# Kernel optimization log

Measured on AMD Instinct MI355X. Metric: run time of the kernel, lower is better.

Reference implementation:

```python
import jax, jax.numpy as jnp
import numpy as np

N_WAY = 5
K_SHOT = 5
SEQ = 196          # patch tokens per image (ViT-S/16 @ 224)
TEMP = 0.0510310363  # similarity temperature ~ 1/sqrt(384)
LR = 0.1
OPT_STEPS = 15


def _normalize(emb):
    # [B, S, D] -> [B*S, D], rows L2-normalized with 1e-8 floor (matches torch.max(norm, 1e-8))
    v = emb.reshape(-1, emb.shape[-1])
    n = jnp.linalg.norm(v, axis=1, keepdims=True)
    return v / jnp.maximum(n, 1e-8)


def _block_mask():
    # block_diag of (SEQ x SEQ) blocks of -100 for each of the n_way*k_shot support images
    return jnp.kron(jnp.eye(N_WAY * K_SHOT, dtype=jnp.float32),
                    jnp.ones((SEQ, SEQ), jnp.float32)) * (-100.0)


def _predict(sup, qry, v, mask):
    # sup: [n_way*k_shot, S, D], qry: [Qb, Qs, D], v: [n_way*k_shot*S]
    S = sup.shape[1]
    Qb, Qs = qry.shape[0], qry.shape[1]
    C = _normalize(sup) @ _normalize(qry).T           # [Ls, Qb*Qs] cosine sims
    if mask is not None:
        C = C + mask
    pred = C + v[:, None]
    pred = pred.reshape(N_WAY, K_SHOT * S, Qb, Qs)
    pred = pred.transpose(0, 1, 3, 2).reshape(N_WAY, K_SHOT * S * Qs, Qb)
    pred = pred / TEMP
    pred = jax.scipy.special.logsumexp(pred, axis=1)  # [n_way, Qb]
    return pred.T                                     # [Qb, n_way]


def _optimize_v(sup_key, sup_query, labels, mask):
    # online SGD on the patch-embedding importance vector v (starts at zero)
    Ls = N_WAY * K_SHOT * sup_key.shape[1]
    B = sup_query.shape[0]

    def loss(v):
        p = _predict(sup_key, sup_query, v, mask)  # [B, n_way]
        logp = jax.nn.log_softmax(p, axis=1)
        return -jnp.mean(logp[jnp.arange(B), labels])

    def step(v, _):
        return v - LR * jax.grad(loss)(v), None

    v, _ = jax.lax.scan(step, jnp.zeros((Ls,), jnp.float32), None, length=OPT_STEPS)
    return v


def setup_inputs() -> dict:
    key = jax.random.key(0)
    k1, k2, k3, k4 = jax.random.split(key, 4)
    return {
        "support_emb_key": jax.random.normal(k1, (N_WAY * K_SHOT, SEQ, 384), jnp.float32),
        "support_emb_query": jax.random.normal(k2, (N_WAY * K_SHOT, SEQ, 384), jnp.float32),
        "query_emb": jax.random.normal(k3, (75, SEQ, 384), jnp.float32),
        "support_labels": jax.random.randint(k4, (N_WAY * K_SHOT,), 0, N_WAY, dtype=jnp.int32),
    }


def reference(support_emb_key, support_emb_query, query_emb, support_labels):
    mask = _block_mask()
    v = _optimize_v(support_emb_key, support_emb_query, support_labels, mask)
    return _predict(support_emb_key, query_emb, v, None)  # [75, n_way]
```

## Files before the change

kernel.cpp:

```cpp
#include <hip/hip_runtime.h>
#include <hip/hip_bf16.h>

#define NW 5
#define KS 5
#define SEQ 196
#define DIM 384
#define NSUP 25
#define NQRY 75
#define NIMG 100
#define LSUP 4900
#define LSUP_PAD 4992
#define QROWS 208
#define BLOCK_W 980
#define OPT_STEPS 15
#define MTILES 39
#define NSUPWG (NSUP * MTILES)
#define NQWG   (NQRY * MTILES)
#define SPIN_LIMIT (1u << 22)

static constexpr float TEMP_F = 0.0510310363f;
static constexpr float INV_T  = 1.0f / TEMP_F;
static constexpr float LR_F   = 0.1f;

typedef short v8s __attribute__((ext_vector_type(8)));
typedef float v4f __attribute__((ext_vector_type(4)));

__device__ inline unsigned short f2bf(float x) {
    unsigned int u = __float_as_uint(x);
    u += 0x7fffu + ((u >> 16) & 1u);
    return (unsigned short)(u >> 16);
}

__device__ __forceinline__ float fresh_f32(float* p) {
    return __hip_atomic_fetch_add(p, 0.0f, __ATOMIC_RELAXED, __HIP_MEMORY_SCOPE_AGENT);
}
__device__ __forceinline__ int fresh_i32(int* p) {
    return __hip_atomic_fetch_add(p, 0, __ATOMIC_RELAXED, __HIP_MEMORY_SCOPE_AGENT);
}
__device__ __forceinline__ unsigned fresh_u32(unsigned* p) {
    return __hip_atomic_fetch_add(p, 0u, __ATOMIC_RELAXED, __HIP_MEMORY_SCOPE_AGENT);
}
__device__ __forceinline__ void agent_store_f32(float* p, float v) {
    __hip_atomic_store(p, v, __ATOMIC_RELAXED, __HIP_MEMORY_SCOPE_AGENT);
}
__device__ __forceinline__ void agent_store_i32(int* p, int v) {
    __hip_atomic_store(p, v, __ATOMIC_RELAXED, __HIP_MEMORY_SCOPE_AGENT);
}

__global__ __launch_bounds__(256) void norm_all(const float* __restrict__ supk,
                                                const float* __restrict__ supq,
                                                const float* __restrict__ qry,
                                                unsigned short* __restrict__ Kb,
                                                unsigned short* __restrict__ Qall) {
    int R = blockIdx.x * 4 + (threadIdx.x >> 6);
    int l = threadIdx.x & 63;
    unsigned short* out;
    const float* in;
    float scale;
    if (R < LSUP_PAD) {
        out = Kb + (size_t)R * DIM;
        if (R >= LSUP) {
            #pragma unroll
            for (int k = 0; k < 6; ++k) out[l + 64 * k] = 0;
            return;
        }
        in = supk + (size_t)R * DIM;
        scale = INV_T;
    } else {
        int i = R - LSUP_PAD;
        int img = i / QROWS;
        int r = i - img * QROWS;
        out = Qall + (size_t)i * DIM;
        if (r >= SEQ) {
            #pragma unroll
            for (int k = 0; k < 6; ++k) out[l + 64 * k] = 0;
            return;
        }
        in = (img < NSUP)
            ? supq + ((size_t)img * SEQ + r) * DIM
            : qry  + ((size_t)(img - NSUP) * SEQ + r) * DIM;
        scale = 1.0f;
    }
    float x[6];
    #pragma unroll
    for (int k = 0; k < 6; ++k) x[k] = in[l + 64 * k];
    float s = 0.f;
    #pragma unroll
    for (int k = 0; k < 6; ++k) s += x[k] * x[k];
    #pragma unroll
    for (int m = 1; m < 64; m <<= 1) s += __shfl_xor(s, m);
    float sc = scale / fmaxf(sqrtf(s), 1e-8f);
    #pragma unroll
    for (int k = 0; k < 6; ++k) out[l + 64 * k] = f2bf(x[k] * sc);
}

#define MT  128
#define NTP 208
#define KCC 64

__device__ __forceinline__ void gload16(const void* g, void* l) {
    __builtin_amdgcn_global_load_lds(
        (__attribute__((address_space(1))) void*)g,
        (__attribute__((address_space(3))) void*)l, 16, 0, 0);
}

template<int IMG_BASE, int NWG, bool SUPPORT>
__device__ __forceinline__ void gemm_body(
    int gid,
    const unsigned short* __restrict__ Kb,
    const unsigned short* __restrict__ Qall,
    float* __restrict__ Rall,
    unsigned* counter,
    unsigned short* Asm, unsigned short* Bsm)
{
    int t = threadIdx.x;

    constexpr int qq = NWG >> 3;
    constexpr int rr = NWG & 7;
    int xcd = gid & 7;
    int sub = gid >> 3;
    int L = (xcd < rr ? xcd * (qq + 1) : rr * (qq + 1) + (xcd - rr) * qq) + sub;
    int img = IMG_BASE + L / MTILES;
    int m_base = (L % MTILES) * MT;

    const unsigned short* Qimg = Qall + (size_t)img * (QROWS * DIM);

    int wv = t >> 6;
    int l  = t & 63;
    int lo = l & 15;
    int hi = l >> 4;
    int mh = (wv >> 1) * 64;
    int nh = wv & 1;

    int srow = l >> 3;
    int skp  = (l & 7) ^ srow;
    const unsigned short* aSrc = Kb   + (size_t)(m_base + wv * 32 + srow) * DIM + skp * 8;
    const unsigned short* bSrc = Qimg + (size_t)srow * DIM + skp * 8;

    v4f acc[4][7];
    #pragma unroll
    for (int m = 0; m < 4; ++m)
        #pragma unroll
        for (int n = 0; n < 7; ++n)
            acc[m][n] = (v4f){0.f, 0.f, 0.f, 0.f};

    for (int kb = 0; kb < DIM; kb += KCC) {
        #pragma unroll
        for (int j = 0; j < 4; ++j)
            gload16(aSrc + (size_t)j * 8 * DIM + kb,
                    Asm + (wv * 32 + j * 8) * KCC);
        #pragma unroll
        for (int jj = 0; jj < 7; ++jj) {
            int j = wv + jj * 4;
            if (j < 26)
                gload16(bSrc + (size_t)j * 8 * DIM + kb,
                        Bsm + j * 8 * KCC);
        }
        __syncthreads();

        const unsigned short* Ar = Asm + (mh + lo) * KCC;
        const unsigned short* Br = Bsm + (nh * 112 + lo) * KCC;
        #pragma unroll
        for (int kk = 0; kk < 2; ++kk) {
            int koff = ((hi + 4 * kk) ^ (lo & 7)) * 8;
            v8s a0 = *(const v8s*)(Ar + koff);
            v8s a1 = *(const v8s*)(Ar + 16 * KCC + koff);
            v8s a2 = *(const v8s*)(Ar + 32 * KCC + koff);
            v8s a3 = *(const v8s*)(Ar + 48 * KCC + koff);
            #pragma unroll
            for (int n = 0; n < 7; ++n) {
                if (nh == 0 || n < 6) {
                    v8s bb = *(const v8s*)(Br + n * 16 * KCC + koff);
                    acc[0][n] = __builtin_amdgcn_mfma_f32_16x16x32_bf16(a0, bb, acc[0][n], 0, 0, 0);
                    acc[1][n] = __builtin_amdgcn_mfma_f32_16x16x32_bf16(a1, bb, acc[1][n], 0, 0, 0);
                    acc[2][n] = __builtin_amdgcn_mfma_f32_16x16x32_bf16(a2, bb, acc[2][n], 0, 0, 0);
                    acc[3][n] = __builtin_amdgcn_mfma_f32_16x16x32_bf16(a3, bb, acc[3][n], 0, 0, 0);
                }
            }
        }
        __syncthreads();
    }

    float s[4][4];
    #pragma unroll
    for (int m = 0; m < 4; ++m)
        #pragma unroll
        for (int j = 0; j < 4; ++j) s[m][j] = 0.f;
    #pragma unroll
    for (int n = 0; n < 7; ++n) {
        if (nh == 0 || n < 6) {
            bool ok = ((nh * 7 + n) * 16 + lo) < SEQ;
            #pragma unroll
            for (int m = 0; m < 4; ++m)
                #pragma unroll
                for (int j = 0; j < 4; ++j)
                    s[m][j] += ok ? __expf(acc[m][n][j]) : 0.f;
        }
    }
    #pragma unroll
    for (int mm = 1; mm < 16; mm <<= 1) {
        #pragma unroll
        for (int m = 0; m < 4; ++m)
            #pragma unroll
            for (int j = 0; j < 4; ++j)
                s[m][j] += __shfl_xor(s[m][j], mm);
    }
    float* rp = (float*)Asm;
    if (lo == 0) {
        #pragma unroll
        for (int m = 0; m < 4; ++m)
            #pragma unroll
            for (int j = 0; j < 4; ++j)
                rp[nh * 128 + mh + m * 16 + hi * 4 + j] = s[m][j];
    }
    __syncthreads();
    if (t < MT) {
        int gr = m_base + t;
        if (gr < LSUP) {
            float o = rp[t] + rp[128 + t];
            if (img < NSUP && (gr / SEQ) == img) o = 0.f;
            if (SUPPORT)
                agent_store_f32(&Rall[(size_t)img * LSUP + gr], o);
            else
                Rall[(size_t)img * LSUP + gr] = o;
        }
    }
    if (SUPPORT) {
        __syncthreads();
        if (t == 0)
            __hip_atomic_fetch_add(counter, 1u, __ATOMIC_RELAXED, __HIP_MEMORY_SCOPE_AGENT);
    }
}

__global__ __launch_bounds__(256, 3) void mega(
    const unsigned short* __restrict__ Kb,
    const unsigned short* __restrict__ Qall,
    float* __restrict__ Rall,
    const int* __restrict__ labels,
    float* __restrict__ Dbuf,
    int* __restrict__ flags,
    unsigned* __restrict__ sdone,
    float* __restrict__ e_out)
{
    __shared__ __align__(16) unsigned short Asm[MT * KCC];
    __shared__ __align__(16) unsigned short Bsm[NTP * KCC];

    int id = blockIdx.x;
    if (id >= NW + NSUPWG) {
        gemm_body<NSUP, NQWG, false>(id - (NW + NSUPWG), Kb, Qall, Rall,
                                     sdone, Asm, Bsm);
        return;
    }
    if (id >= NW) {
        gemm_body<0, NSUPWG, true>(id - NW, Kb, Qall, Rall,
                                   sdone, Asm, Bsm);
        return;
    }

    float* sh  = (float*)Asm;
    float* red = sh;
    float* cfs = sh + 100;
    float* Dsm = sh + 128;
    float* myD = sh + 256;
    int*   lsm = (int*)(sh + 288);

    int w = id;
    int t = threadIdx.x;
    int wave = t >> 6, lane = t & 63;

    if (t == 0) {
        unsigned spins = 0;
        while (fresh_u32(sdone) < (unsigned)NSUPWG && ++spins < SPIN_LIMIT)
            __builtin_amdgcn_s_sleep(8);
    }
    __syncthreads();

    float Rv[4][NSUP];
    #pragma unroll
    for (int b = 0; b < NSUP; ++b) {
        const float* Rb = Rall + (size_t)b * LSUP + w * BLOCK_W;
        Rv[0][b] = Rb[t];
        Rv[1][b] = Rb[t + 256];
        Rv[2][b] = Rb[t + 512];
        Rv[3][b] = (t < BLOCK_W - 768) ? Rb[t + 768] : 0.f;
    }
    if (t < NSUP) lsm[t] = labels[t];

    float e0 = 1.f, e1 = 1.f, e2 = 1.f, e3 = 1.f;
    float v0 = 0.f, v1 = 0.f, v2 = 0.f, v3 = 0.f;

    auto pushD = [&](int step) {
        float part[NSUP];
        #pragma unroll
        for (int b = 0; b < NSUP; ++b)
            part[b] = e0 * Rv[0][b] + e1 * Rv[1][b] + e2 * Rv[2][b] + e3 * Rv[3][b];
        #pragma unroll
        for (int b = 0; b < NSUP; ++b) {
            #pragma unroll
            for (int m = 32; m; m >>= 1) part[b] += __shfl_xor(part[b], m);
        }
        if (lane == 0) {
            #pragma unroll
            for (int b = 0; b < NSUP; ++b) red[wave * NSUP + b] = part[b];
        }
        __syncthreads();
        if (t < NSUP) {
            float s = red[t] + red[NSUP + t] + red[2 * NSUP + t] + red[3 * NSUP + t];
            myD[t] = s;
            agent_store_f32(&Dbuf[(step * NW + w) * 32 + t], s);
        }
        __syncthreads();
        if (t == 0)
            agent_store_i32(&flags[w * 32], step + 1);
    };

    pushD(0);

    for (int s = 0; s < OPT_STEPS; ++s) {
        if (wave == 0) {
            unsigned spins = 0;
            for (;;) {
                int f = (lane < NW) ? fresh_i32(&flags[lane * 32]) : 0x7fffffff;
                if (__all(f >= s + 1)) break;
                if (++spins >= SPIN_LIMIT) break;
                __builtin_amdgcn_s_sleep(1);
            }
        }
        __syncthreads();
        if (t < 125) {
            int wp = t / 25, b = t - wp * 25;
            float dv = (wp == w) ? myD[b]
                                 : fresh_f32(&Dbuf[(s * NW + wp) * 32 + b]);
            Dsm[b * 5 + wp] = dv;
        }
        __syncthreads();
        if (t < NSUP) {
            float Dsum = 0.f, Dw = 1.f;
            #pragma unroll
            for (int ww = 0; ww < NW; ++ww) {
                float d = Dsm[t * 5 + ww];
                Dsum += d;
                if (ww == w) Dw = d;
            }
            cfs[t] = ((Dw / Dsum) - (w == lsm[t] ? 1.f : 0.f)) * (INV_T / 25.f) / Dw;
        }
        __syncthreads();
        float g0 = 0.f, g1 = 0.f, g2 = 0.f, g3 = 0.f;
        #pragma unroll
        for (int b = 0; b < NSUP; ++b) {
            float c = cfs[b];
            g0 += c * Rv[0][b];
            g1 += c * Rv[1][b];
            g2 += c * Rv[2][b];
            g3 += c * Rv[3][b];
        }
        v0 -= LR_F * e0 * g0; e0 = __expf(v0 * INV_T);
        v1 -= LR_F * e1 * g1; e1 = __expf(v1 * INV_T);
        v2 -= LR_F * e2 * g2; e2 = __expf(v2 * INV_T);
        v3 -= LR_F * e3 * g3; e3 = __expf(v3 * INV_T);
        __syncthreads();
        if (s + 1 < OPT_STEPS) pushD(s + 1);
    }

    float* eo = e_out + w * BLOCK_W;
    eo[t]       = e0;
    eo[t + 256] = e1;
    eo[t + 512] = e2;
    if (t < BLOCK_W - 768) eo[t + 768] = e3;
}

__global__ __launch_bounds__(256) void final_pred(const float* __restrict__ Rall,
                                                  const float* __restrict__ e_out,
                                                  float* __restrict__ out) {
    __shared__ float ws[4];
    int blk = blockIdx.x;
    int qb = blk / 5, w = blk % 5;
    const float* R  = Rall + (size_t)(NSUP + qb) * LSUP + w * BLOCK_W;
    const float* eb = e_out + w * BLOCK_W;
    int t = threadIdx.x;
    float p = 0.f;
    for (int i = t; i < BLOCK_W; i += 256) p += eb[i] * R[i];
    #pragma unroll
    for (int m = 32; m; m >>= 1) p += __shfl_xor(p, m);
    if ((t & 63) == 0) ws[t >> 6] = p;
    __syncthreads();
    if (t == 0) out[blk] = logf(ws[0] + ws[1] + ws[2] + ws[3]);
}

extern "C" void kernel_launch(void* const* d_in, const int* in_sizes, int n_in,
                              void* d_out, int out_size, void* d_ws, size_t ws_size,
                              hipStream_t stream) {
    const float* sup_key = (const float*)d_in[0];
    const float* sup_qry = (const float*)d_in[1];
    const float* qry     = (const float*)d_in[2];
    const int*   labels  = (const int*)d_in[3];
    float* out = (float*)d_out;

    char* ws = (char*)d_ws;
    size_t off = 0;
    auto take = [&](size_t bytes) {
        char* p = ws + off;
        off = (off + bytes + 255) & ~(size_t)255;
        return p;
    };
    unsigned short* Kb   = (unsigned short*)take((size_t)LSUP_PAD * DIM * 2);
    unsigned short* Qall = (unsigned short*)take((size_t)NIMG * QROWS * DIM * 2);
    float*          Rall = (float*)take((size_t)NIMG * LSUP * 4);
    float*          Dbuf = (float*)take((size_t)16 * NW * 32 * 4);
    float*          eout = (float*)take((size_t)LSUP * 4);
    int*            fl   = (int*)take(256 * 4);
    int*            flags = fl;
    unsigned*       sdone = (unsigned*)(fl + 192);

    hipMemsetAsync(Dbuf, 0, (size_t)16 * NW * 32 * 4, stream);
    hipMemsetAsync(fl, 0, 256 * 4, stream);

    norm_all<<<(LSUP_PAD + NIMG * QROWS) / 4, 256, 0, stream>>>(
        sup_key, sup_qry, qry, Kb, Qall);

    mega<<<NW + NSUPWG + NQWG, 256, 0, stream>>>(
        Kb, Qall, Rall, labels, Dbuf, flags, sdone, eout);

    final_pred<<<NQRY * NW, 256, 0, stream>>>(Rall, eout, out);
}
```

Baseline: 237.2 us.

## Fold workspace zeroing into norm kernel and compute initial D in GEMM epilogue

Removes the two hipMemsetAsync calls by having an extra block of norm_all zero the Dbuf/flags region. The support GEMM epilogue now accumulates per-block row sums into D0 with LDS then global atomics, so the optimizer blocks skip the initial pushD and its first flag wait. The Dbuf layout becomes [step][b][w] so each step reads one contiguous 125-entry slice, and flags are packed without padding. This trades the memset launches and one cross-block round trip for extra atomics in the GEMM epilogue and possible false sharing on the packed flags.

Result: faster. 225.5 us (-4.9%).

```diff
diff --git a/kernel.cpp b/kernel.cpp
--- a/kernel.cpp
+++ b/kernel.cpp
@@ -16,6 +16,7 @@
 #define MTILES 39
 #define NSUPWG (NSUP * MTILES)
 #define NQWG   (NQRY * MTILES)
+#define NORMWG ((LSUP_PAD + NIMG * QROWS) / 4)
 #define SPIN_LIMIT (1u << 22)
 
 static constexpr float TEMP_F = 0.0510310363f;
@@ -51,7 +52,13 @@
                                                 const float* __restrict__ supq,
                                                 const float* __restrict__ qry,
                                                 unsigned short* __restrict__ Kb,
-                                                unsigned short* __restrict__ Qall) {
+                                                unsigned short* __restrict__ Qall,
+                                                float* __restrict__ zbuf) {
+    if (blockIdx.x == NORMWG) {
+        for (int i = threadIdx.x; i < (OPT_STEPS + 1) * 125 + 64; i += 256)
+            zbuf[i] = 0.f;
+        return;
+    }
     int R = blockIdx.x * 4 + (threadIdx.x >> 6);
     int l = threadIdx.x & 63;
     unsigned short* out;
@@ -110,6 +117,7 @@
     const unsigned short* __restrict__ Kb,
     const unsigned short* __restrict__ Qall,
     float* __restrict__ Rall,
+    float* __restrict__ D0,
     unsigned* counter,
     unsigned short* Asm, unsigned short* Bsm)
 {
@@ -213,19 +221,29 @@
             for (int j = 0; j < 4; ++j)
                 rp[nh * 128 + mh + m * 16 + hi * 4 + j] = s[m][j];
     }
+    if (SUPPORT && t == 0) { rp[256] = 0.f; rp[257] = 0.f; }
     __syncthreads();
+    int w0 = m_base / BLOCK_W;
     if (t < MT) {
         int gr = m_base + t;
         if (gr < LSUP) {
             float o = rp[t] + rp[128 + t];
             if (img < NSUP && (gr / SEQ) == img) o = 0.f;
-            if (SUPPORT)
+            if (SUPPORT) {
                 agent_store_f32(&Rall[(size_t)img * LSUP + gr], o);
-            else
+                atomicAdd(&rp[256 + (gr / BLOCK_W - w0)], o);
+            } else {
                 Rall[(size_t)img * LSUP + gr] = o;
+            }
         }
     }
     if (SUPPORT) {
+        __syncthreads();
+        if (t < 2) {
+            int w = w0 + t;
+            if (w < NW && w * BLOCK_W < m_base + MT)
+                atomicAdd(&D0[img * 5 + w], rp[256 + t]);
+        }
         __syncthreads();
         if (t == 0)
             __hip_atomic_fetch_add(counter, 1u, __ATOMIC_RELAXED, __HIP_MEMORY_SCOPE_AGENT);
@@ -237,7 +255,7 @@
     const unsigned short* __restrict__ Qall,
     float* __restrict__ Rall,
     const int* __restrict__ labels,
-    float* __restrict__ Dbuf,
+    float* __restrict__ Dbufs,
     int* __restrict__ flags,
     unsigned* __restrict__ sdone,
     float* __restrict__ e_out)
@@ -248,12 +266,12 @@
     int id = blockIdx.x;
     if (id >= NW + NSUPWG) {
         gemm_body<NSUP, NQWG, false>(id - (NW + NSUPWG), Kb, Qall, Rall,
-                                     sdone, Asm, Bsm);
+                                     Dbufs, sdone, Asm, Bsm);
         return;
     }
     if (id >= NW) {
         gemm_body<0, NSUPWG, true>(id - NW, Kb, Qall, Rall,
-                                   sdone, Asm, Bsm);
+                                   Dbufs, sdone, Asm, Bsm);
         return;
     }
 
@@ -261,8 +279,7 @@
     float* red = sh;
     float* cfs = sh + 100;
     float* Dsm = sh + 128;
-    float* myD = sh + 256;
-    int*   lsm = (int*)(sh + 288);
+    int*   lsm = (int*)(sh + 256);
 
     int w = id;
     int t = threadIdx.x;
@@ -306,33 +323,26 @@
         __syncthreads();
         if (t < NSUP) {
             float s = red[t] + red[NSUP + t] + red[2 * NSUP + t] + red[3 * NSUP + t];
-            myD[t] = s;
-            agent_store_f32(&Dbuf[(step * NW + w) * 32 + t], s);
+            agent_store_f32(&Dbufs[step * 125 + t * 5 + w], s);
         }
         __syncthreads();
         if (t == 0)
-            agent_store_i32(&flags[w * 32], step + 1);
+            agent_store_i32(&flags[w], step);
     };
 
-    pushD(0);
-
     for (int s = 0; s < OPT_STEPS; ++s) {
-        if (wave == 0) {
+        if (s > 0 && wave == 0) {
             unsigned spins = 0;
             for (;;) {
-                int f = (lane < NW) ? fresh_i32(&flags[lane * 32]) : 0x7fffffff;
-                if (__all(f >= s + 1)) break;
+                int f = (lane < NW) ? fresh_i32(&flags[lane]) : 0x7fffffff;
+                if (__all(f >= s)) break;
                 if (++spins >= SPIN_LIMIT) break;
                 __builtin_amdgcn_s_sleep(1);
             }
         }
         __syncthreads();
-        if (t < 125) {
-            int wp = t / 25, b = t - wp * 25;
-            float dv = (wp == w) ? myD[b]
-                                 : fresh_f32(&Dbuf[(s * NW + wp) * 32 + b]);
-            Dsm[b * 5 + wp] = dv;
-        }
+        if (t < 125)
+            Dsm[t] = fresh_f32(&Dbufs[s * 125 + t]);
         __syncthreads();
         if (t < NSUP) {
             float Dsum = 0.f, Dw = 1.f;
@@ -406,17 +416,13 @@
     unsigned short* Kb   = (unsigned short*)take((size_t)LSUP_PAD * DIM * 2);
     unsigned short* Qall = (unsigned short*)take((size_t)NIMG * QROWS * DIM * 2);
     float*          Rall = (float*)take((size_t)NIMG * LSUP * 4);
-    float*          Dbuf = (float*)take((size_t)16 * NW * 32 * 4);
+    float*          Dbuf = (float*)take(((size_t)(OPT_STEPS + 1) * 125 + 64) * 4);
     float*          eout = (float*)take((size_t)LSUP * 4);
-    int*            fl   = (int*)take(256 * 4);
-    int*            flags = fl;
-    unsigned*       sdone = (unsigned*)(fl + 192);
-
-    hipMemsetAsync(Dbuf, 0, (size_t)16 * NW * 32 * 4, stream);
-    hipMemsetAsync(fl, 0, 256 * 4, stream);
-
-    norm_all<<<(LSUP_PAD + NIMG * QROWS) / 4, 256, 0, stream>>>(
-        sup_key, sup_qry, qry, Kb, Qall);
+    int*            flags = (int*)(Dbuf + (OPT_STEPS + 1) * 125);
+    unsigned*       sdone = (unsigned*)(flags + 16);
+
+    norm_all<<<NORMWG + 1, 256, 0, stream>>>(
+        sup_key, sup_qry, qry, Kb, Qall, Dbuf);
 
     mega<<<NW + NSUPWG + NQWG, 256, 0, stream>>>(
         Kb, Qall, Rall, labels, Dbuf, flags, sdone, eout);
```
